# Optimization experiments

Hardware: AMD Instinct MI355X
Metric: run time of the kernel (lower is better)

Reference implementation:

```python
import jax, jax.numpy as jnp
import numpy as np
from jax import lax

VOCAB, EMBED_DIM, NUM_TAGS = 50000, 300, 16
BATCH, SEQ = 64, 512


def setup_inputs() -> dict:
    key = jax.random.key(0)
    k0, k1, k2, k3, k4 = jax.random.split(key, 5)
    text = jax.random.randint(k0, (BATCH, SEQ), 0, VOCAB)
    tags = jax.random.randint(k1, (BATCH, SEQ), 0, NUM_TAGS)
    embed_table = jax.random.normal(k2, (VOCAB, EMBED_DIM), jnp.float32) * 0.02
    W = jax.random.normal(k3, (EMBED_DIM, NUM_TAGS), jnp.float32) * 0.05
    b = jnp.zeros((NUM_TAGS,), jnp.float32)
    trans = jax.random.uniform(k4, (NUM_TAGS, NUM_TAGS), jnp.float32)
    return {"text": text, "tags": tags, "embed_table": embed_table, "W": W, "b": b, "trans": trans}


def crf_log_likelihood(probs, tags, lens, trans):
    # probs: [B,S,T] unary potentials; tags: [B,S] int; lens: [B]; trans: [T,T]
    B, S, T = probs.shape
    t_idx = jnp.arange(S)
    mask = (t_idx[None, :] < lens[:, None])  # [B,S] valid positions

    # --- gold sequence score ---
    unary = jnp.take_along_axis(probs, tags[..., None], axis=2)[..., 0]  # [B,S]
    unary_score = jnp.sum(unary * mask, axis=1)
    btrans = trans[tags[:, :-1], tags[:, 1:]]            # [B,S-1]
    bmask = mask[:, 1:]                                   # transition t->t+1 valid iff t+1 < len
    binary_score = jnp.sum(btrans * bmask, axis=1)

    # --- forward algorithm (log partition) ---
    alpha0 = probs[:, 0]                                  # [B,T]
    emits = jnp.moveaxis(probs[:, 1:], 0, 1)              # [S-1,B,T]
    ms = jnp.moveaxis(mask[:, 1:], 0, 1)                  # [S-1,B]

    def step(alpha, inp):
        emit, m = inp
        new = jax.nn.logsumexp(alpha[:, :, None] + trans[None, :, :], axis=1) + emit
        return jnp.where(m[:, None], new, alpha), None

    alpha, _ = lax.scan(step, alpha0, (emits, ms))
    log_norm = jax.nn.logsumexp(alpha, axis=-1)           # [B]
    return unary_score + binary_score - log_norm


def reference(text, tags, embed_table, W, b, trans):
    # dropout is identity in eval/reference mode
    text_lens = jnp.sum((text != 0).astype(jnp.int32), axis=1)  # [B]
    probs = embed_table[text] @ W + b                            # [B,S,T]
    log_likelihood = crf_log_likelihood(probs, tags, text_lens, trans)
    return probs, text_lens, log_likelihood
```

## Files before the change

kernel.cpp:

```cpp
#include <hip/hip_runtime.h>
#include <hip/hip_bf16.h>

#define VOCAB 50000
#define ED    300
#define NT    16
#define BB    64
#define SS    512

#define LOG2E 1.4426950408889634f
#define LN2   0.6931471805599453f
#define WSTR  308

__global__ __launch_bounds__(256) void probs_kernel(const int* __restrict__ text,
                                                    const float* __restrict__ emb,
                                                    const float* __restrict__ W,
                                                    const float* __restrict__ bias,
                                                    float* __restrict__ out_probs) {
  __shared__ float wt[NT * WSTR];

  const int tid = threadIdx.x;
  const int lane = tid & 63, wave = tid >> 6;
  const int r = lane >> 4, t = lane & 15;
  const int row = blockIdx.x * 16 + wave * 4 + r;

  for (int e = tid; e < ED * NT; e += 256) {
    int d = e >> 4, tt = e & 15;
    wt[tt * WSTR + d] = W[e];
  }

  const int tok = text[row];
  const float4* erow = (const float4*)(emb + (size_t)tok * ED);
  float acc = bias[t];

  float4 A[8];
#pragma unroll
  for (int i = 0; i < 8; ++i) A[i] = erow[i];

  __syncthreads();

  const float4* w4 = (const float4*)(wt + t * WSTR);
#pragma unroll
  for (int c = 0; c < 75; ++c) {
    float4 e = A[c & 7];
    if (c < 67) A[c & 7] = erow[c + 8];
    float4 w = w4[c];
    acc = fmaf(e.x, w.x, acc);
    acc = fmaf(e.y, w.y, acc);
    acc = fmaf(e.z, w.z, acc);
    acc = fmaf(e.w, w.w, acc);
  }
  out_probs[(size_t)row * NT + t] = acc;
}

template <int CTRL>
__device__ __forceinline__ float dppmov(float x) {
  int xi = __float_as_int(x);
  return __int_as_float(
      __builtin_amdgcn_update_dpp(xi, xi, CTRL, 0xF, 0xF, false));
}

__device__ __forceinline__ float crf_step(float g, float pe, const float E[16]) {
  float gn, h, m, c, a1, a2, a3;
  asm("s_nop 1\n\t"
      "v_mov_b32_dpp %[h], %[g] row_half_mirror row_mask:0xf bank_mask:0xf\n\t"
      "v_mov_b32_dpp %[m], %[g] row_mirror row_mask:0xf bank_mask:0xf\n\t"
      "v_mul_f32 %[gn], %[g], %[e0]\n\t"
      "v_fmac_f32_dpp %[gn], %[g], %[e1] quad_perm:[1,0,3,2] row_mask:0xf bank_mask:0xf\n\t"
      "v_fmac_f32_dpp %[gn], %[g], %[e2] quad_perm:[2,3,0,1] row_mask:0xf bank_mask:0xf\n\t"
      "v_fmac_f32_dpp %[gn], %[g], %[e3] quad_perm:[3,2,1,0] row_mask:0xf bank_mask:0xf\n\t"
      "v_mov_b32_dpp %[c], %[m] row_half_mirror row_mask:0xf bank_mask:0xf\n\t"
      "v_mul_f32 %[a1], %[h], %[e7]\n\t"
      "v_fmac_f32_dpp %[a1], %[h], %[e6] quad_perm:[1,0,3,2] row_mask:0xf bank_mask:0xf\n\t"
      "v_fmac_f32_dpp %[a1], %[h], %[e5] quad_perm:[2,3,0,1] row_mask:0xf bank_mask:0xf\n\t"
      "v_fmac_f32_dpp %[a1], %[h], %[e4] quad_perm:[3,2,1,0] row_mask:0xf bank_mask:0xf\n\t"
      "v_mul_f32 %[a2], %[m], %[e15]\n\t"
      "v_fmac_f32_dpp %[a2], %[m], %[e14] quad_perm:[1,0,3,2] row_mask:0xf bank_mask:0xf\n\t"
      "v_fmac_f32_dpp %[a2], %[m], %[e13] quad_perm:[2,3,0,1] row_mask:0xf bank_mask:0xf\n\t"
      "v_fmac_f32_dpp %[a2], %[m], %[e12] quad_perm:[3,2,1,0] row_mask:0xf bank_mask:0xf\n\t"
      "v_mul_f32 %[a3], %[c], %[e8]\n\t"
      "v_fmac_f32_dpp %[a3], %[c], %[e9] quad_perm:[1,0,3,2] row_mask:0xf bank_mask:0xf\n\t"
      "v_fmac_f32_dpp %[a3], %[c], %[e10] quad_perm:[2,3,0,1] row_mask:0xf bank_mask:0xf\n\t"
      "v_fmac_f32_dpp %[a3], %[c], %[e11] quad_perm:[3,2,1,0] row_mask:0xf bank_mask:0xf\n\t"
      "v_add_f32 %[gn], %[gn], %[a1]\n\t"
      "v_add_f32 %[a2], %[a2], %[a3]\n\t"
      "v_add_f32 %[gn], %[gn], %[a2]\n\t"
      "v_mul_f32 %[gn], %[gn], %[pe]"
      : [gn] "=&v"(gn), [h] "=&v"(h), [m] "=&v"(m), [c] "=&v"(c),
        [a1] "=&v"(a1), [a2] "=&v"(a2), [a3] "=&v"(a3)
      : [g] "v"(g), [pe] "v"(pe),
        [e0] "v"(E[0]), [e1] "v"(E[1]), [e2] "v"(E[2]), [e3] "v"(E[3]),
        [e4] "v"(E[4]), [e5] "v"(E[5]), [e6] "v"(E[6]), [e7] "v"(E[7]),
        [e8] "v"(E[8]), [e9] "v"(E[9]), [e10] "v"(E[10]), [e11] "v"(E[11]),
        [e12] "v"(E[12]), [e13] "v"(E[13]), [e14] "v"(E[14]), [e15] "v"(E[15]));
  return gn;
}

__global__ __launch_bounds__(64) void crf_kernel(const int* __restrict__ text,
                                                 const int* __restrict__ tags,
                                                 const float* __restrict__ trans,
                                                 const float* __restrict__ probs,
                                                 float* __restrict__ out_lens,
                                                 float* __restrict__ out_ll) {
  __shared__ float lps[(SS + 1) * NT];
  __shared__ int tgs[SS];
  __shared__ float trs[256];

  const int tid = threadIdx.x;
  const int j = tid & 15;
  const int b = blockIdx.x;

  {
    const float4* p4 = (const float4*)(probs + (size_t)b * SS * NT);
    float4* l4 = (float4*)lps;
#pragma unroll
    for (int i = 0; i < 32; ++i) {
      float4 v = p4[tid + 64 * i];
      v.x *= LOG2E; v.y *= LOG2E; v.z *= LOG2E; v.w *= LOG2E;
      l4[tid + 64 * i] = v;
    }
    const int4* t4 = (const int4*)(tags + b * SS);
    int4* lt = (int4*)tgs;
#pragma unroll
    for (int i = 0; i < 2; ++i) lt[tid + 64 * i] = t4[tid + 64 * i];
    for (int i = tid; i < 256; i += 64) trs[i] = trans[i];
  }
  __syncthreads();

  const int* tx = text + b * SS;
  int cnt = 0;
#pragma unroll
  for (int k = 0; k < 8; ++k) cnt += (tx[tid + 64 * k] != 0) ? 1 : 0;
  for (int off = 32; off > 0; off >>= 1) cnt += __shfl_xor(cnt, off, 64);
  const int len = cnt;
  if (tid == 0) out_lens[b] = (float)len;

  float su = 0.f, sb = 0.f;
#pragma unroll
  for (int it = 0; it < 8; ++it) {
    const int s = tid + 64 * it;
    if (s < len) {
      int t1 = tgs[s];
      su += lps[s * NT + t1];
      if (s >= 1) sb += trs[tgs[s - 1] * 16 + t1];
    }
  }
  float sc = fmaf(su, LN2, sb);
  for (int off = 32; off > 0; off >>= 1) sc += __shfl_xor(sc, off, 64);

  float E[16];
#pragma unroll
  for (int k = 0; k < 16; ++k) E[k] = __expf(trs[((j ^ k) << 4) + j]) * 0.03125f;

  float g = exp2f(lps[j]);
  float K2 = 0.f;

  const int T = (len > 0) ? len - 1 : 0;
  const int nfull = T >> 4;
  const int rem = T & 15;

  float raw[16];
#pragma unroll
  for (int c = 0; c < 16; ++c) raw[c] = lps[(1 + c) * NT + j];

  int s0 = 1;
  for (int blk = 0; blk < nfull; ++blk) {
#pragma unroll
    for (int c = 0; c < 16; ++c) {
      float pe = exp2f(raw[c]);
      raw[c] = lps[(s0 + 16 + c) * NT + j];
      g = crf_step(g, pe, E);
    }
    if ((blk & 3) == 3) {
      float mx = g;
      mx = fmaxf(mx, dppmov<0xB1>(mx));
      mx = fmaxf(mx, dppmov<0x4E>(mx));
      mx = fmaxf(mx, dppmov<0x141>(mx));
      mx = fmaxf(mx, dppmov<0x140>(mx));
      float rr = 1.0f / mx;
      K2 -= __log2f(rr);
      g *= rr;
    }
    s0 += 16;
  }
  for (int c = 0; c < rem; ++c) {
    float pe = exp2f(raw[c]);
    g = crf_step(g, pe, E);
  }

  float x = g;
  x += dppmov<0xB1>(x);
  x += dppmov<0x4E>(x);
  x += dppmov<0x141>(x);
  x += dppmov<0x140>(x);
  float log_norm = LN2 * (K2 + 5.0f * (float)T + __log2f(x));
  if (tid == 0) out_ll[b] = sc - log_norm;
}

extern "C" void kernel_launch(void* const* d_in, const int* in_sizes, int n_in,
                              void* d_out, int out_size, void* d_ws, size_t ws_size,
                              hipStream_t stream) {
  const int* text = (const int*)d_in[0];
  const int* tags = (const int*)d_in[1];
  const float* emb = (const float*)d_in[2];
  const float* W = (const float*)d_in[3];
  const float* bias = (const float*)d_in[4];
  const float* trans = (const float*)d_in[5];

  float* out = (float*)d_out;
  float* out_probs = out;
  float* out_lens = out + BB * SS * NT;
  float* out_ll = out + BB * SS * NT + BB;

  probs_kernel<<<(BB * SS) / 16, 256, 0, stream>>>(text, emb, W, bias, out_probs);
  crf_kernel<<<BB, 64, 0, stream>>>(text, tags, trans, out_probs, out_lens, out_ll);
}
```

Measured before the change: 152.0 us.

## Fuse probs and CRF kernels with a grid-wide atomic counter barrier

Merges the embedding-projection kernel and the CRF forward kernel into one launch. The first 64 blocks go on to run the CRF recurrence after spinning on a global atomic counter until all 2048 blocks have written their probs. They then read probs straight from global memory instead of staging them in LDS. This removes one kernel launch and the inter-kernel gap, and lets the tag/transition setup overlap with the tail of the projection. The cost is a memset launch, a spin-wait that relies on all blocks being co-resident or scheduled in order, and a serial recurrence that now reads global memory inside its loop.

```diff
diff --git a/kernel.cpp b/kernel.cpp
--- a/kernel.cpp
+++ b/kernel.cpp
@@ -10,47 +10,7 @@
 #define LOG2E 1.4426950408889634f
 #define LN2   0.6931471805599453f
 #define WSTR  308
-
-__global__ __launch_bounds__(256) void probs_kernel(const int* __restrict__ text,
-                                                    const float* __restrict__ emb,
-                                                    const float* __restrict__ W,
-                                                    const float* __restrict__ bias,
-                                                    float* __restrict__ out_probs) {
-  __shared__ float wt[NT * WSTR];
-
-  const int tid = threadIdx.x;
-  const int lane = tid & 63, wave = tid >> 6;
-  const int r = lane >> 4, t = lane & 15;
-  const int row = blockIdx.x * 16 + wave * 4 + r;
-
-  for (int e = tid; e < ED * NT; e += 256) {
-    int d = e >> 4, tt = e & 15;
-    wt[tt * WSTR + d] = W[e];
-  }
-
-  const int tok = text[row];
-  const float4* erow = (const float4*)(emb + (size_t)tok * ED);
-  float acc = bias[t];
-
-  float4 A[8];
-#pragma unroll
-  for (int i = 0; i < 8; ++i) A[i] = erow[i];
-
-  __syncthreads();
-
-  const float4* w4 = (const float4*)(wt + t * WSTR);
-#pragma unroll
-  for (int c = 0; c < 75; ++c) {
-    float4 e = A[c & 7];
-    if (c < 67) A[c & 7] = erow[c + 8];
-    float4 w = w4[c];
-    acc = fmaf(e.x, w.x, acc);
-    acc = fmaf(e.y, w.y, acc);
-    acc = fmaf(e.z, w.z, acc);
-    acc = fmaf(e.w, w.w, acc);
-  }
-  out_probs[(size_t)row * NT + t] = acc;
-}
+#define NBLK  2048
 
 template <int CTRL>
 __device__ __forceinline__ float dppmov(float x) {
@@ -95,63 +55,94 @@
   return gn;
 }
 
-__global__ __launch_bounds__(64) void crf_kernel(const int* __restrict__ text,
-                                                 const int* __restrict__ tags,
-                                                 const float* __restrict__ trans,
-                                                 const float* __restrict__ probs,
-                                                 float* __restrict__ out_lens,
-                                                 float* __restrict__ out_ll) {
-  __shared__ float lps[(SS + 1) * NT];
-  __shared__ int tgs[SS];
-  __shared__ float trs[256];
+__global__ __launch_bounds__(256) void fused_kernel(const int* __restrict__ text,
+                                                    const int* __restrict__ tags,
+                                                    const float* __restrict__ emb,
+                                                    const float* __restrict__ W,
+                                                    const float* __restrict__ bias,
+                                                    const float* __restrict__ trans,
+                                                    float* __restrict__ out_probs,
+                                                    float* __restrict__ out_lens,
+                                                    float* __restrict__ out_ll,
+                                                    int* __restrict__ cnt) {
+  __shared__ float wt[NT * WSTR];
 
   const int tid = threadIdx.x;
+  const int lane = tid & 63, wave = tid >> 6;
+  const int r = lane >> 4, t = lane & 15;
+  const int row = blockIdx.x * 16 + wave * 4 + r;
+
+  for (int e = tid; e < ED * NT; e += 256) {
+    int d = e >> 4, tt = e & 15;
+    wt[tt * WSTR + d] = W[e];
+  }
+
+  const int tok = text[row];
+  const float4* erow = (const float4*)(emb + (size_t)tok * ED);
+  float acc = bias[t];
+
+  float4 A[8];
+#pragma unroll
+  for (int i = 0; i < 8; ++i) A[i] = erow[i];
+
+  __syncthreads();
+
+  const float4* w4 = (const float4*)(wt + t * WSTR);
+#pragma unroll
+  for (int c = 0; c < 75; ++c) {
+    float4 e = A[c & 7];
+    if (c < 67) A[c & 7] = erow[c + 8];
+    float4 w = w4[c];
+    acc = fmaf(e.x, w.x, acc);
+    acc = fmaf(e.y, w.y, acc);
+    acc = fmaf(e.z, w.z, acc);
+    acc = fmaf(e.w, w.w, acc);
+  }
+  __builtin_nontemporal_store(acc, out_probs + (size_t)row * NT + t);
+
+  __syncthreads();
+  if (tid == 0)
+    __hip_atomic_fetch_add(cnt, 1, __ATOMIC_RELAXED, __HIP_MEMORY_SCOPE_AGENT);
+
+  const int b = blockIdx.x;
+  if (b >= BB || tid >= 64) return;
+
   const int j = tid & 15;
-  const int b = blockIdx.x;
-
-  {
-    const float4* p4 = (const float4*)(probs + (size_t)b * SS * NT);
-    float4* l4 = (float4*)lps;
-#pragma unroll
-    for (int i = 0; i < 32; ++i) {
-      float4 v = p4[tid + 64 * i];
-      v.x *= LOG2E; v.y *= LOG2E; v.z *= LOG2E; v.w *= LOG2E;
-      l4[tid + 64 * i] = v;
-    }
-    const int4* t4 = (const int4*)(tags + b * SS);
-    int4* lt = (int4*)tgs;
-#pragma unroll
-    for (int i = 0; i < 2; ++i) lt[tid + 64 * i] = t4[tid + 64 * i];
-    for (int i = tid; i < 256; i += 64) trs[i] = trans[i];
-  }
-  __syncthreads();
 
   const int* tx = text + b * SS;
-  int cnt = 0;
-#pragma unroll
-  for (int k = 0; k < 8; ++k) cnt += (tx[tid + 64 * k] != 0) ? 1 : 0;
-  for (int off = 32; off > 0; off >>= 1) cnt += __shfl_xor(cnt, off, 64);
-  const int len = cnt;
+  int cz = 0;
+#pragma unroll
+  for (int k = 0; k < 8; ++k) cz += (tx[tid + 64 * k] != 0) ? 1 : 0;
+  for (int off = 32; off > 0; off >>= 1) cz += __shfl_xor(cz, off, 64);
+  const int len = cz;
   if (tid == 0) out_lens[b] = (float)len;
 
-  float su = 0.f, sb = 0.f;
+  const int* tg = tags + b * SS;
+  int tgv[8];
+  float sb = 0.f;
 #pragma unroll
   for (int it = 0; it < 8; ++it) {
     const int s = tid + 64 * it;
-    if (s < len) {
-      int t1 = tgs[s];
-      su += lps[s * NT + t1];
-      if (s >= 1) sb += trs[tgs[s - 1] * 16 + t1];
+    tgv[it] = tg[s];
+    if (s >= 1 && s < len) sb += trans[tg[s - 1] * 16 + tgv[it]];
+  }
+
+  float E[16];
+#pragma unroll
+  for (int k = 0; k < 16; ++k) E[k] = __expf(trans[((j ^ k) << 4) + j]) * 0.03125f;
+
+  {
+    unsigned guard = 0;
+    while (__hip_atomic_load(cnt, __ATOMIC_RELAXED, __HIP_MEMORY_SCOPE_AGENT) < NBLK) {
+      __builtin_amdgcn_s_sleep(4);
+      if (++guard > (1u << 22)) break;
     }
-  }
-  float sc = fmaf(su, LN2, sb);
-  for (int off = 32; off > 0; off >>= 1) sc += __shfl_xor(sc, off, 64);
-
-  float E[16];
-#pragma unroll
-  for (int k = 0; k < 16; ++k) E[k] = __expf(trs[((j ^ k) << 4) + j]) * 0.03125f;
-
-  float g = exp2f(lps[j]);
+    __threadfence();
+  }
+
+  const float* pb = out_probs + (size_t)b * SS * NT;
+
+  float g = exp2f(pb[j] * LOG2E);
   float K2 = 0.f;
 
   const int T = (len > 0) ? len - 1 : 0;
@@ -160,14 +151,14 @@
 
   float raw[16];
 #pragma unroll
-  for (int c = 0; c < 16; ++c) raw[c] = lps[(1 + c) * NT + j];
+  for (int c = 0; c < 16; ++c) raw[c] = pb[(1 + c) * NT + j] * LOG2E;
 
   int s0 = 1;
   for (int blk = 0; blk < nfull; ++blk) {
 #pragma unroll
     for (int c = 0; c < 16; ++c) {
       float pe = exp2f(raw[c]);
-      raw[c] = lps[(s0 + 16 + c) * NT + j];
+      raw[c] = pb[(s0 + 16 + c) * NT + j] * LOG2E;
       g = crf_step(g, pe, E);
     }
     if ((blk & 3) == 3) {
@@ -187,6 +178,15 @@
     g = crf_step(g, pe, E);
   }
 
+  float su = 0.f;
+#pragma unroll
+  for (int it = 0; it < 8; ++it) {
+    const int s = tid + 64 * it;
+    if (s < len) su += pb[s * NT + tgv[it]];
+  }
+  float sc = su + sb;
+  for (int off = 32; off > 0; off >>= 1) sc += __shfl_xor(sc, off, 64);
+
   float x = g;
   x += dppmov<0xB1>(x);
   x += dppmov<0x4E>(x);
@@ -211,6 +211,9 @@
   float* out_lens = out + BB * SS * NT;
   float* out_ll = out + BB * SS * NT + BB;
 
-  probs_kernel<<<(BB * SS) / 16, 256, 0, stream>>>(text, emb, W, bias, out_probs);
-  crf_kernel<<<BB, 64, 0, stream>>>(text, tags, trans, out_probs, out_lens, out_ll);
-}
+  int* cnt = (int*)d_ws;
+  hipMemsetAsync(d_ws, 0, 64, stream);
+
+  fused_kernel<<<NBLK, 256, 0, stream>>>(text, tags, emb, W, bias, trans,
+                                         out_probs, out_lens, out_ll, cnt);
+}
```

Result: slower. 195.1 us (+28.3%).
